# Performance work log

Measured on AMD Instinct MI355X. Metric: run time of the kernel, lower is better.

## Reference

```python
import jax, jax.numpy as jnp
import numpy as np
import math

ALPHA = 2.0  # spikingjelly surrogate.ATan default alpha
TAU = 2.0
MEM_DECAY = math.exp(-1.0 / TAU)
ADAPT_STRENGTH = 0.1
TARGET_RATE = 0.02
THR_MIN = 0.5
N_HEAD = 4

@jax.custom_vjp
def spike_fn(x):
    # Heaviside forward, ATan surrogate backward
    return (x >= 0.0).astype(x.dtype)

def _spike_fwd(x):
    return spike_fn(x), x

def _spike_bwd(x, g):
    return (g * (ALPHA / 2.0) / (1.0 + (jnp.pi / 2.0 * ALPHA * x) ** 2),)

spike_fn.defvjp(_spike_fwd, _spike_bwd)

def lif_step(x, v_mem, thr):
    # thr is a buffer in torch (updated under no_grad): no grad flows to it
    thr_c = jax.lax.stop_gradient(thr)
    v_pot = v_mem * MEM_DECAY + x
    spike = spike_fn(v_pot - thr_c)
    v_new = v_pot * (1.0 - jax.lax.stop_gradient(spike))
    err = jax.lax.stop_gradient(jnp.mean(spike)) - TARGET_RATE
    thr_new = jnp.maximum(thr_c + ADAPT_STRENGTH * err, THR_MIN)
    return spike, v_new, thr_new

def setup_inputs() -> dict:
    key = jax.random.key(0)
    ks = jax.random.split(key, 10)
    B, T, S, D, DS = 8, 16, 256, 512, 64
    x = jax.random.normal(ks[0], (B, T, S, D), jnp.float32)
    A = jax.random.normal(ks[1], (DS, DS), jnp.float32)
    C = jax.random.normal(ks[2], (D, DS), jnp.float32)
    s = 1.0 / math.sqrt(DS)
    Wq = jax.random.uniform(ks[3], (DS, DS), jnp.float32, -s, s)
    bq = jax.random.uniform(ks[4], (DS,), jnp.float32, -s, s)
    sd = 1.0 / math.sqrt(D)
    Wkv = jax.random.uniform(ks[5], (2 * DS, D), jnp.float32, -sd, sd)
    bkv = jax.random.uniform(ks[6], (2 * DS,), jnp.float32, -sd, sd)
    Wo = jax.random.uniform(ks[7], (DS, DS), jnp.float32, -s, s)
    bo = jax.random.uniform(ks[8], (DS,), jnp.float32, -s, s)
    thr_s0 = jnp.full((DS,), 1.0, jnp.float32)
    thr_o0 = jnp.full((D,), 1.0, jnp.float32)
    return {"x": x, "A": A, "C": C, "Wq": Wq, "bq": bq, "Wkv": Wkv,
            "bkv": bkv, "Wo": Wo, "bo": bo, "thr_s0": thr_s0, "thr_o0": thr_o0}

def reference(x, A, C, Wq, bq, Wkv, bkv, Wo, bo, thr_s0, thr_o0):
    B, T, S, D = x.shape
    DS = A.shape[0]
    H = N_HEAD
    dh = DS // H
    N = B * S
    scale = 1.0 / math.sqrt(dh)
    h0 = jnp.zeros((B, S, DS), x.dtype)
    sv0 = jnp.zeros((B, S, DS), x.dtype)
    ov0 = jnp.zeros((B, S, D), x.dtype)

    def step(carry, x_t):
        h, sv, ov, ts, to = carry
        state_transition = h @ A.T                              # (B,S,DS)
        q = (h @ Wq.T + bq).reshape(N, H, dh).transpose(1, 0, 2)   # (H,N,dh)
        kv = x_t @ Wkv.T + bkv                                  # (B,S,2*DS)
        k = kv[..., :DS].reshape(N, H, dh).transpose(1, 0, 2)   # (H,N,dh)
        v = kv[..., DS:].reshape(N, H, dh).transpose(1, 0, 2)   # (H,N,dh)
        scores = jnp.einsum('hnd,hmd->hnm', q, k) * scale       # (H,N,N)
        w = jax.nn.softmax(scores, axis=-1)
        att = jnp.einsum('hnm,hmd->hnd', w, v)                  # (H,N,dh)
        att = att.transpose(1, 0, 2).reshape(B, S, DS)
        state_update = state_transition + att @ Wo.T + bo
        h2, sv2, ts2 = lif_step(state_update, sv, ts)
        output_potential = h2 @ C.T                             # (B,S,D)
        out, ov2, to2 = lif_step(output_potential, ov, to)
        return (h2, sv2, ov2, ts2, to2), out

    _, outs = jax.lax.scan(step, (h0, sv0, ov0, thr_s0, thr_o0),
                           jnp.moveaxis(x, 1, 0))               # outs: (T,B,S,D)
    return jnp.moveaxis(outs, 0, 1)                             # (B,T,S,D)
```

## Files before the change

### kernel.cpp

```cpp
#include <hip/hip_runtime.h>
#include <math.h>


#define NTOK   2048
#define TSTEPS 16
#define NSPLIT 32

#define MEMDECAY ((float)0.6065306597126334)
#define SCALE    0.25f

#define OFF_KV   ((size_t)0)
#define OFF_PACC ((size_t)4194304)
#define OFF_OV   ((size_t)8388608)
#define OFF_H    ((size_t)9437184)
#define OFF_SV   ((size_t)9568256)
#define OFF_Q    ((size_t)9699328)
#define OFF_PM   ((size_t)9830400)
#define OFF_PL   ((size_t)10092544)
#define OFF_CT   ((size_t)10354688)
#define OFF_CNT  ((size_t)10387456)
#define OFF_WT   ((size_t)10387488)

__global__ __launch_bounds__(256) void init_kernel(const float* __restrict__ bq,
                                                   const float* __restrict__ C,
                                                   const float* __restrict__ Wkv,
                                                   float* __restrict__ ws) {
  int i = blockIdx.x * 256 + threadIdx.x;
  if (i < 327680) {
    float4 z = {0.f, 0.f, 0.f, 0.f};
    ((float4*)(ws + OFF_OV))[i] = z;
    return;
  }
  i -= 327680;
  if (i < 131072) { ws[OFF_Q + i] = bq[i & 63]; return; }
  i -= 131072;
  if (i < 32768) {
    int k = i >> 9, c = i & 511;
    ws[OFF_CT + i] = C[c * 64 + k];
    return;
  }
  i -= 32768;
  if (i < 65536) {
    int k = i >> 7, o = i & 127;
    ws[OFF_WT + i] = Wkv[o * 512 + k];
    return;
  }
  i -= 65536;
  if (i < 32) ((int*)(ws + OFF_CNT))[i] = 0;
}

__global__ __launch_bounds__(256) void kv_gemm_kernel(const float* __restrict__ x,
                                                      const float* __restrict__ wkt,
                                                      const float* __restrict__ bkv,
                                                      float* __restrict__ ws) {
  __shared__ float xs[64 * 68];
  __shared__ float wt[64 * 136];
  const int tid = threadIdx.x;
  const int mbase = blockIdx.x * 64;
  const int rg = tid >> 4;
  const int cg = tid & 15;

  float acc[4][8];
#pragma unroll
  for (int i = 0; i < 4; ++i)
#pragma unroll
    for (int j = 0; j < 8; ++j) acc[i][j] = 0.f;

  for (int kt = 0; kt < 8; ++kt) {
    const int kb = kt * 64;
#pragma unroll
    for (int p = 0; p < 4; ++p) {
      int e = tid + p * 256;
      int r = e >> 4, kq = e & 15;
      int row = mbase + r;
      int t_ = row >> 11, n = row & 2047;
      int b = n >> 8, s = n & 255;
      float4 v = *(const float4*)(x + (size_t)((b * 16 + t_) * 256 + s) * 512 + kb + kq * 4);
      *(float4*)(xs + r * 68 + kq * 4) = v;
    }
#pragma unroll
    for (int p = 0; p < 8; ++p) {
      int e = tid + p * 256;
      int k = e >> 5, cq = e & 31;
      float4 v = *(const float4*)(wkt + (size_t)(kb + k) * 128 + cq * 4);
      *(float4*)(wt + k * 136 + cq * 4) = v;
    }
    __syncthreads();
#pragma unroll 2
    for (int kq = 0; kq < 16; ++kq) {
      float4 a0 = *(const float4*)(xs + (rg * 4 + 0) * 68 + kq * 4);
      float4 a1 = *(const float4*)(xs + (rg * 4 + 1) * 68 + kq * 4);
      float4 a2 = *(const float4*)(xs + (rg * 4 + 2) * 68 + kq * 4);
      float4 a3 = *(const float4*)(xs + (rg * 4 + 3) * 68 + kq * 4);
      const float* ap[4] = {(const float*)&a0, (const float*)&a1,
                            (const float*)&a2, (const float*)&a3};
#pragma unroll
      for (int kk = 0; kk < 3 + 1; ++kk) {
        const float* wp = wt + (kq * 4 + kk) * 136 + cg * 8;
        float4 b0 = *(const float4*)(wp);
        float4 b1 = *(const float4*)(wp + 4);
#pragma unroll
        for (int i = 0; i < 4; ++i) {
          float av = ap[i][kk];
          acc[i][0] += av * b0.x; acc[i][1] += av * b0.y;
          acc[i][2] += av * b0.z; acc[i][3] += av * b0.w;
          acc[i][4] += av * b1.x; acc[i][5] += av * b1.y;
          acc[i][6] += av * b1.z; acc[i][7] += av * b1.w;
        }
      }
    }
    __syncthreads();
  }
  float4 bb0 = *(const float4*)(bkv + cg * 8);
  float4 bb1 = *(const float4*)(bkv + cg * 8 + 4);
  float* kvout = ws + OFF_KV;
#pragma unroll
  for (int i = 0; i < 4; ++i) {
    float* op = kvout + (size_t)(mbase + rg * 4 + i) * 128 + cg * 8;
    float4 v0; v0.x = acc[i][0] + bb0.x; v0.y = acc[i][1] + bb0.y;
    v0.z = acc[i][2] + bb0.z; v0.w = acc[i][3] + bb0.w;
    float4 v1; v1.x = acc[i][4] + bb1.x; v1.y = acc[i][5] + bb1.y;
    v1.z = acc[i][6] + bb1.z; v1.w = acc[i][7] + bb1.w;
    *(float4*)(op) = v0;
    *(float4*)(op + 4) = v1;
  }
}

__device__ __forceinline__ void attp_body(int blk, int tid, int t,
                                          const float* __restrict__ kvbase,
                                          const float* __restrict__ qbuf,
                                          float* __restrict__ pm,
                                          float* __restrict__ pl,
                                          float* __restrict__ pacc,
                                          float* smem) {
  const int head = blk & 3;
  const int qt = (blk >> 2) & 3;
  const int sp = blk >> 4;
  float* kl = smem;
  float* vl = smem + 1024;
  const float* kvt = kvbase + (size_t)t * NTOK * 128;
  {
    int key = tid >> 2, dq = tid & 3;
    const float* base = kvt + (size_t)(sp * 64 + key) * 128 + head * 16;
    float4 kk = ((const float4*)base)[dq];
    float4 vv = ((const float4*)(base + 64))[dq];
    ((float4*)kl)[key * 4 + dq] = kk;
    ((float4*)vl)[key * 4 + dq] = vv;
  }
  const int i0 = qt * 512 + tid;
  const int i1 = i0 + 256;
  float q0[16], q1[16];
  {
    const float4* qp0 = (const float4*)(qbuf + (size_t)i0 * 64 + head * 16);
    const float4* qp1 = (const float4*)(qbuf + (size_t)i1 * 64 + head * 16);
#pragma unroll
    for (int r = 0; r < 4; ++r) {
      float4 a = qp0[r];
      q0[4 * r] = a.x; q0[4 * r + 1] = a.y; q0[4 * r + 2] = a.z; q0[4 * r + 3] = a.w;
      float4 b = qp1[r];
      q1[4 * r] = b.x; q1[4 * r + 1] = b.y; q1[4 * r + 2] = b.z; q1[4 * r + 3] = b.w;
    }
  }
  __syncthreads();
  float m0 = -INFINITY, l0 = 0.f, m1 = -INFINITY, l1 = 0.f;
  float acc0[16], acc1[16];
#pragma unroll
  for (int d = 0; d < 16; ++d) { acc0[d] = 0.f; acc1[d] = 0.f; }

#pragma unroll
  for (int ch = 0; ch < 4; ++ch) {
    float sc0[16], sc1[16];
#pragma unroll
    for (int j = 0; j < 16; ++j) {
      const float* kp = kl + (ch * 16 + j) * 16;
      float s0 = 0.f, s1 = 0.f;
#pragma unroll
      for (int d = 0; d < 16; ++d) { float kv_ = kp[d]; s0 += q0[d] * kv_; s1 += q1[d] * kv_; }
      sc0[j] = s0 * SCALE; sc1[j] = s1 * SCALE;
    }
    float mb0 = sc0[0], mb1 = sc1[0];
#pragma unroll
    for (int j = 1; j < 16; ++j) { mb0 = fmaxf(mb0, sc0[j]); mb1 = fmaxf(mb1, sc1[j]); }
    float mn0 = fmaxf(m0, mb0), mn1 = fmaxf(m1, mb1);
    float r0 = expf(m0 - mn0), r1 = expf(m1 - mn1);
    l0 *= r0; l1 *= r1;
#pragma unroll
    for (int d = 0; d < 16; ++d) { acc0[d] *= r0; acc1[d] *= r1; }
#pragma unroll
    for (int j = 0; j < 16; ++j) {
      float w0 = expf(sc0[j] - mn0), w1 = expf(sc1[j] - mn1);
      l0 += w0; l1 += w1; sc0[j] = w0; sc1[j] = w1;
    }
#pragma unroll
    for (int j = 0; j < 16; ++j) {
      const float* vp = vl + (ch * 16 + j) * 16;
      float w0 = sc0[j], w1 = sc1[j];
#pragma unroll
      for (int d = 0; d < 16; ++d) { float vv = vp[d]; acc0[d] += w0 * vv; acc1[d] += w1 * vv; }
    }
    m0 = mn0; m1 = mn1;
  }
  const int pbase = (head * NSPLIT + sp) * NTOK;
  pm[pbase + i0] = m0; pm[pbase + i1] = m1;
  pl[pbase + i0] = l0; pl[pbase + i1] = l1;
  float4* pa0 = (float4*)(pacc + (size_t)(pbase + i0) * 16);
  float4* pa1 = (float4*)(pacc + (size_t)(pbase + i1) * 16);
#pragma unroll
  for (int r = 0; r < 4; ++r) {
    float4 v0; v0.x = acc0[4 * r]; v0.y = acc0[4 * r + 1]; v0.z = acc0[4 * r + 2]; v0.w = acc0[4 * r + 3];
    pa0[r] = v0;
    float4 v1; v1.x = acc1[4 * r]; v1.y = acc1[4 * r + 1]; v1.z = acc1[4 * r + 2]; v1.w = acc1[4 * r + 3];
    pa1[r] = v1;
  }
}

__global__ __launch_bounds__(256) void attp_kernel(int t, float* __restrict__ ws) {
  __shared__ float smem[2048];
  attp_body(blockIdx.x, threadIdx.x, t, ws + OFF_KV, ws + OFF_Q,
            ws + OFF_PM, ws + OFF_PL, ws + OFF_PACC, smem);
}

__global__ __launch_bounds__(256) void combine_lifs_kernel(
    int t, const float* __restrict__ A, const float* __restrict__ Wq,
    const float* __restrict__ bq, const float* __restrict__ Wo,
    const float* __restrict__ bo, const float* __restrict__ thr_s0,
    float* __restrict__ ws) {
  __shared__ float As[64 * 68], Wqs[64 * 68], Wos[64 * 68];
  __shared__ float att_s[4][64], hv_s[4][64], sp_s[4][64];
  __shared__ int scnt;
  const int tid = threadIdx.x;
#pragma unroll
  for (int p = 0; p < 4; ++p) {
    int e = tid + p * 256;
    int c = e >> 4, kq = e & 15;
    *(float4*)(As + c * 68 + kq * 4)  = *(const float4*)(A + c * 64 + kq * 4);
    *(float4*)(Wqs + c * 68 + kq * 4) = *(const float4*)(Wq + c * 64 + kq * 4);
    *(float4*)(Wos + c * 68 + kq * 4) = *(const float4*)(Wo + c * 64 + kq * 4);
  }
  if (tid == 0) scnt = 0;

  const float* pm = ws + OFF_PM;
  const float* pl = ws + OFF_PL;
  const float* pacc = ws + OFF_PACC;
  float* h = ws + OFF_H;
  float* sv = ws + OFF_SV;
  float* qb = ws + OFF_Q;
  int* cnt = (int*)(ws + OFF_CNT);

  const int lane = tid & 63, w = tid >> 6;
  const int n = blockIdx.x * 4 + w;
  const int head = lane >> 4, d = lane & 15;
  const int pb = head * NSPLIT * NTOK + n;

  float mstar = -INFINITY;
  for (int s = 0; s < NSPLIT; ++s) mstar = fmaxf(mstar, pm[pb + s * NTOK]);
  float lst = 0.f, av = 0.f;
  for (int s = 0; s < NSPLIT; ++s) {
    float e = expf(pm[pb + s * NTOK] - mstar);
    lst += e * pl[pb + s * NTOK];
    av += e * pacc[(size_t)(pb + s * NTOK) * 16 + d];
  }
  att_s[w][lane] = av / lst;
  float hv = h[n * 64 + lane];
  hv_s[w][lane] = hv;
  __syncthreads();

  const float* Ar = As + lane * 68;
  const float* Wor = Wos + lane * 68;
  float st = 0.f, wo = 0.f;
#pragma unroll
  for (int kq = 0; kq < 16; ++kq) {
    float4 wa = *(const float4*)(Ar + kq * 4);
    float4 wb = *(const float4*)(Wor + kq * 4);
    float4 hb = *(const float4*)(&hv_s[w][kq * 4]);
    float4 ab = *(const float4*)(&att_s[w][kq * 4]);
    st += hb.x * wa.x; st += hb.y * wa.y; st += hb.z * wa.z; st += hb.w * wa.w;
    wo += ab.x * wb.x; wo += ab.y * wb.y; wo += ab.z * wb.z; wo += ab.w * wb.w;
  }
  float su = st + wo + bo[lane];

  float thr = thr_s0[0];
  const float inv = 1.0f / 131072.0f;
  for (int i = 0; i < t; ++i) {
    float mean = (float)cnt[i] * inv;
    thr = fmaxf(thr + 0.1f * (mean - 0.02f), 0.5f);
  }
  float svo = sv[n * 64 + lane];
  float vpot = svo * MEMDECAY + su;
  float spk = (vpot >= thr) ? 1.f : 0.f;
  h[n * 64 + lane] = spk;
  sv[n * 64 + lane] = vpot * (1.f - spk);
  sp_s[w][lane] = spk;
  unsigned long long sm = __ballot(spk > 0.5f);

  const float* Wqr = Wqs + lane * 68;
  float qv = 0.f;
#pragma unroll
  for (int kq = 0; kq < 16; ++kq) {
    float4 wq = *(const float4*)(Wqr + kq * 4);
    float4 sb = *(const float4*)(&sp_s[w][kq * 4]);
    qv += sb.x * wq.x; qv += sb.y * wq.y; qv += sb.z * wq.z; qv += sb.w * wq.w;
  }
  qb[n * 64 + lane] = qv + bq[lane];

  if (lane == 0) atomicAdd(&scnt, __popcll(sm));
  __syncthreads();
  if (tid == 0) atomicAdd(&cnt[t], scnt);
}

__global__ __launch_bounds__(256) void fused_out_attp_kernel(
    int t, const float* __restrict__ thr_o0, float* __restrict__ out,
    float* __restrict__ ws) {
  __shared__ float smem[64 * 66 + 64 * 68];
  __shared__ int scnt;
  const int blk = blockIdx.x;
  if (blk >= 256) {
    attp_body(blk - 256, threadIdx.x, t + 1, ws + OFF_KV, ws + OFF_Q,
              ws + OFF_PM, ws + OFF_PL, ws + OFF_PACC, smem);
    return;
  }
  const int tid = threadIdx.x;
  const int nt = blk >> 3;
  const int ct = blk & 7;
  float* hs = smem;
  float* cts = smem + 64 * 66;
  const float* h = ws + OFF_H;
  const float* Ct = ws + OFF_CT;
  float* ov = ws + OFF_OV;
  int* cnt = (int*)(ws + OFF_CNT);

#pragma unroll
  for (int p = 0; p < 4; ++p) {
    int e = tid + p * 256;
    int r = e >> 4, kq = e & 15;
    float4 v = *(const float4*)(h + (size_t)(nt * 64 + r) * 64 + kq * 4);
    float* dd = hs + r * 66 + kq * 4;
    dd[0] = v.x; dd[1] = v.y; dd[2] = v.z; dd[3] = v.w;
  }
#pragma unroll
  for (int p = 0; p < 4; ++p) {
    int e = tid + p * 256;
    int k = e >> 4, cq = e & 15;
    float4 v = *(const float4*)(Ct + (size_t)k * 512 + ct * 64 + cq * 4);
    float* dd = cts + k * 68 + cq * 4;
    dd[0] = v.x; dd[1] = v.y; dd[2] = v.z; dd[3] = v.w;
  }
  if (tid == 0) scnt = 0;
  __syncthreads();

  const int tr = tid >> 4, tc = tid & 15;
  float acc[4][4];
#pragma unroll
  for (int i = 0; i < 4; ++i)
#pragma unroll
    for (int j = 0; j < 4; ++j) acc[i][j] = 0.f;

#pragma unroll 4
  for (int k = 0; k < 64; ++k) {
    float hv[4];
#pragma unroll
    for (int i = 0; i < 4; ++i) hv[i] = hs[(tr + i * 16) * 66 + k];
    const float* cp = cts + k * 68 + tc * 4;
    float c0 = cp[0], c1 = cp[1], c2 = cp[2], c3 = cp[3];
#pragma unroll
    for (int i = 0; i < 4; ++i) {
      acc[i][0] += hv[i] * c0;
      acc[i][1] += hv[i] * c1;
      acc[i][2] += hv[i] * c2;
      acc[i][3] += hv[i] * c3;
    }
  }

  float thr = thr_o0[0];
  const float inv = 1.0f / 1048576.0f;
  for (int i = 0; i < t; ++i) {
    float mean = (float)cnt[16 + i] * inv;
    thr = fmaxf(thr + 0.1f * (mean - 0.02f), 0.5f);
  }

  int mycount = 0;
#pragma unroll
  for (int i = 0; i < 4; ++i) {
    int n = nt * 64 + tr + i * 16;
    int b = n >> 8, s = n & 255;
    size_t coff = (size_t)ct * 64 + tc * 4;
    float* ovp = ov + (size_t)n * 512 + coff;
    float* outp = out + ((size_t)(b * 16 + t) * 256 + s) * 512 + coff;
    float4 o = *(float4*)ovp;
    float v0 = o.x * MEMDECAY + acc[i][0];
    float v1 = o.y * MEMDECAY + acc[i][1];
    float v2 = o.z * MEMDECAY + acc[i][2];
    float v3 = o.w * MEMDECAY + acc[i][3];
    float s0 = (v0 >= thr) ? 1.f : 0.f;
    float s1 = (v1 >= thr) ? 1.f : 0.f;
    float s2 = (v2 >= thr) ? 1.f : 0.f;
    float s3 = (v3 >= thr) ? 1.f : 0.f;
    float4 sp; sp.x = s0; sp.y = s1; sp.z = s2; sp.w = s3;
    *(float4*)outp = sp;
    float4 nv; nv.x = v0 * (1.f - s0); nv.y = v1 * (1.f - s1);
    nv.z = v2 * (1.f - s2); nv.w = v3 * (1.f - s3);
    *(float4*)ovp = nv;
    mycount += (int)(s0 + s1 + s2 + s3);
  }
  atomicAdd(&scnt, mycount);
  __syncthreads();
  if (tid == 0) atomicAdd(&cnt[16 + t], scnt);
}

extern "C" void kernel_launch(void* const* d_in, const int* in_sizes, int n_in,
                              void* d_out, int out_size, void* d_ws, size_t ws_size,
                              hipStream_t stream) {
  const float* x    = (const float*)d_in[0];
  const float* A    = (const float*)d_in[1];
  const float* C    = (const float*)d_in[2];
  const float* Wq   = (const float*)d_in[3];
  const float* bq   = (const float*)d_in[4];
  const float* Wkv  = (const float*)d_in[5];
  const float* bkv  = (const float*)d_in[6];
  const float* Wo   = (const float*)d_in[7];
  const float* bo   = (const float*)d_in[8];
  const float* th_s = (const float*)d_in[9];
  const float* th_o = (const float*)d_in[10];
  float* out = (float*)d_out;
  float* ws = (float*)d_ws;

  init_kernel<<<dim3(2177), dim3(256), 0, stream>>>(bq, C, Wkv, ws);
  kv_gemm_kernel<<<dim3(512), dim3(256), 0, stream>>>(x, ws + OFF_WT, bkv, ws);
  attp_kernel<<<dim3(512), dim3(256), 0, stream>>>(0, ws);
  for (int t = 0; t < TSTEPS; ++t) {
    combine_lifs_kernel<<<dim3(512), dim3(256), 0, stream>>>(t, A, Wq, bq, Wo, bo, th_s, ws);
    int g = (t < TSTEPS - 1) ? 768 : 256;
    fused_out_attp_kernel<<<dim3(g), dim3(256), 0, stream>>>(t, th_o, out, ws);
  }
}
```

Measured before the change: 1.002 ms.

## Halve attention key splits, one query per thread, reorder KV projection columns

The split-KV attention partial kernel now uses 16 splits of 128 keys instead of 32 splits of 64 keys. Each thread handles one query instead of two, with 8 query tiles instead of 4, so the grid size stays the same. This halves the partial max/sum/accumulator traffic written per step and read by the combine kernel, at the cost of double the key length per block and twice the shared memory. The KV projection kernel also changes which output columns each thread owns, writing K and V halves with cg*4 strides, and the combine loops are unrolled.

```diff
diff --git a/kernel.cpp b/kernel.cpp
--- a/kernel.cpp
+++ b/kernel.cpp
@@ -4,22 +4,22 @@
 
 #define NTOK   2048
 #define TSTEPS 16
-#define NSPLIT 32
+#define NSPLIT 16
 
 #define MEMDECAY ((float)0.6065306597126334)
 #define SCALE    0.25f
 
 #define OFF_KV   ((size_t)0)
 #define OFF_PACC ((size_t)4194304)
-#define OFF_OV   ((size_t)8388608)
-#define OFF_H    ((size_t)9437184)
-#define OFF_SV   ((size_t)9568256)
-#define OFF_Q    ((size_t)9699328)
-#define OFF_PM   ((size_t)9830400)
-#define OFF_PL   ((size_t)10092544)
-#define OFF_CT   ((size_t)10354688)
-#define OFF_CNT  ((size_t)10387456)
-#define OFF_WT   ((size_t)10387488)
+#define OFF_OV   ((size_t)6291456)
+#define OFF_H    ((size_t)7340032)
+#define OFF_SV   ((size_t)7471104)
+#define OFF_Q    ((size_t)7602176)
+#define OFF_PM   ((size_t)7733248)
+#define OFF_PL   ((size_t)7864320)
+#define OFF_CT   ((size_t)7995392)
+#define OFF_CNT  ((size_t)8028160)
+#define OFF_WT   ((size_t)8028192)
 
 __global__ __launch_bounds__(256) void init_kernel(const float* __restrict__ bq,
                                                    const float* __restrict__ C,
@@ -95,10 +95,10 @@
       const float* ap[4] = {(const float*)&a0, (const float*)&a1,
                             (const float*)&a2, (const float*)&a3};
 #pragma unroll
-      for (int kk = 0; kk < 3 + 1; ++kk) {
-        const float* wp = wt + (kq * 4 + kk) * 136 + cg * 8;
-        float4 b0 = *(const float4*)(wp);
-        float4 b1 = *(const float4*)(wp + 4);
+      for (int kk = 0; kk < 4; ++kk) {
+        const float* wp = wt + (kq * 4 + kk) * 136;
+        float4 b0 = *(const float4*)(wp + cg * 4);
+        float4 b1 = *(const float4*)(wp + 64 + cg * 4);
 #pragma unroll
         for (int i = 0; i < 4; ++i) {
           float av = ap[i][kk];
@@ -111,18 +111,18 @@
     }
     __syncthreads();
   }
-  float4 bb0 = *(const float4*)(bkv + cg * 8);
-  float4 bb1 = *(const float4*)(bkv + cg * 8 + 4);
+  float4 bb0 = *(const float4*)(bkv + cg * 4);
+  float4 bb1 = *(const float4*)(bkv + 64 + cg * 4);
   float* kvout = ws + OFF_KV;
 #pragma unroll
   for (int i = 0; i < 4; ++i) {
-    float* op = kvout + (size_t)(mbase + rg * 4 + i) * 128 + cg * 8;
+    float* op = kvout + (size_t)(mbase + rg * 4 + i) * 128;
     float4 v0; v0.x = acc[i][0] + bb0.x; v0.y = acc[i][1] + bb0.y;
     v0.z = acc[i][2] + bb0.z; v0.w = acc[i][3] + bb0.w;
     float4 v1; v1.x = acc[i][4] + bb1.x; v1.y = acc[i][5] + bb1.y;
     v1.z = acc[i][6] + bb1.z; v1.w = acc[i][7] + bb1.w;
-    *(float4*)(op) = v0;
-    *(float4*)(op + 4) = v1;
+    *(float4*)(op + cg * 4) = v0;
+    *(float4*)(op + 64 + cg * 4) = v1;
   }
 }
 
@@ -134,88 +134,81 @@
                                           float* __restrict__ pacc,
                                           float* smem) {
   const int head = blk & 3;
-  const int qt = (blk >> 2) & 3;
-  const int sp = blk >> 4;
+  const int qt = (blk >> 2) & 7;
+  const int sp = blk >> 5;
   float* kl = smem;
-  float* vl = smem + 1024;
+  float* vl = smem + 2048;
   const float* kvt = kvbase + (size_t)t * NTOK * 128;
-  {
-    int key = tid >> 2, dq = tid & 3;
-    const float* base = kvt + (size_t)(sp * 64 + key) * 128 + head * 16;
-    float4 kk = ((const float4*)base)[dq];
-    float4 vv = ((const float4*)(base + 64))[dq];
-    ((float4*)kl)[key * 4 + dq] = kk;
-    ((float4*)vl)[key * 4 + dq] = vv;
-  }
-  const int i0 = qt * 512 + tid;
-  const int i1 = i0 + 256;
-  float q0[16], q1[16];
+#pragma unroll
+  for (int p = 0; p < 2; ++p) {
+    int e = tid + p * 256;
+    int key = e >> 2, dq = e & 3;
+    const float* base = kvt + (size_t)(sp * 128 + key) * 128 + head * 16;
+    ((float4*)kl)[key * 4 + dq] = ((const float4*)base)[dq];
+    ((float4*)vl)[key * 4 + dq] = ((const float4*)(base + 64))[dq];
+  }
+  const int i0 = qt * 256 + tid;
+  float q0[16];
   {
     const float4* qp0 = (const float4*)(qbuf + (size_t)i0 * 64 + head * 16);
-    const float4* qp1 = (const float4*)(qbuf + (size_t)i1 * 64 + head * 16);
 #pragma unroll
     for (int r = 0; r < 4; ++r) {
       float4 a = qp0[r];
       q0[4 * r] = a.x; q0[4 * r + 1] = a.y; q0[4 * r + 2] = a.z; q0[4 * r + 3] = a.w;
-      float4 b = qp1[r];
-      q1[4 * r] = b.x; q1[4 * r + 1] = b.y; q1[4 * r + 2] = b.z; q1[4 * r + 3] = b.w;
     }
   }
   __syncthreads();
-  float m0 = -INFINITY, l0 = 0.f, m1 = -INFINITY, l1 = 0.f;
-  float acc0[16], acc1[16];
-#pragma unroll
-  for (int d = 0; d < 16; ++d) { acc0[d] = 0.f; acc1[d] = 0.f; }
-
-#pragma unroll
-  for (int ch = 0; ch < 4; ++ch) {
-    float sc0[16], sc1[16];
+  float m0 = -INFINITY, l0 = 0.f;
+  float acc0[16];
+#pragma unroll
+  for (int d = 0; d < 16; ++d) acc0[d] = 0.f;
+
+  for (int ch = 0; ch < 8; ++ch) {
+    float sc0[16];
 #pragma unroll
     for (int j = 0; j < 16; ++j) {
       const float* kp = kl + (ch * 16 + j) * 16;
-      float s0 = 0.f, s1 = 0.f;
-#pragma unroll
-      for (int d = 0; d < 16; ++d) { float kv_ = kp[d]; s0 += q0[d] * kv_; s1 += q1[d] * kv_; }
-      sc0[j] = s0 * SCALE; sc1[j] = s1 * SCALE;
-    }
-    float mb0 = sc0[0], mb1 = sc1[0];
-#pragma unroll
-    for (int j = 1; j < 16; ++j) { mb0 = fmaxf(mb0, sc0[j]); mb1 = fmaxf(mb1, sc1[j]); }
-    float mn0 = fmaxf(m0, mb0), mn1 = fmaxf(m1, mb1);
-    float r0 = expf(m0 - mn0), r1 = expf(m1 - mn1);
-    l0 *= r0; l1 *= r1;
-#pragma unroll
-    for (int d = 0; d < 16; ++d) { acc0[d] *= r0; acc1[d] *= r1; }
+      float s0 = 0.f;
+#pragma unroll
+      for (int d = 0; d < 16; ++d) s0 += q0[d] * kp[d];
+      sc0[j] = s0 * SCALE;
+    }
+    float mb0 = sc0[0];
+#pragma unroll
+    for (int j = 1; j < 16; ++j) mb0 = fmaxf(mb0, sc0[j]);
+    float mn0 = fmaxf(m0, mb0);
+    float r0 = expf(m0 - mn0);
+    l0 *= r0;
+#pragma unroll
+    for (int d = 0; d < 16; ++d) acc0[d] *= r0;
 #pragma unroll
     for (int j = 0; j < 16; ++j) {
-      float w0 = expf(sc0[j] - mn0), w1 = expf(sc1[j] - mn1);
-      l0 += w0; l1 += w1; sc0[j] = w0; sc1[j] = w1;
+      float w0 = expf(sc0[j] - mn0);
+      l0 += w0; sc0[j] = w0;
     }
 #pragma unroll
     for (int j = 0; j < 16; ++j) {
       const float* vp = vl + (ch * 16 + j) * 16;
-      float w0 = sc0[j], w1 = sc1[j];
-#pragma unroll
-      for (int d = 0; d < 16; ++d) { float vv = vp[d]; acc0[d] += w0 * vv; acc1[d] += w1 * vv; }
-    }
-    m0 = mn0; m1 = mn1;
+      float w0 = sc0[j];
+#pragma unroll
+      for (int d = 0; d < 16; ++d) acc0[d] += w0 * vp[d];
+    }
+    m0 = mn0;
   }
   const int pbase = (head * NSPLIT + sp) * NTOK;
-  pm[pbase + i0] = m0; pm[pbase + i1] = m1;
-  pl[pbase + i0] = l0; pl[pbase + i1] = l1;
+  pm[pbase + i0] = m0;
+  pl[pbase + i0] = l0;
   float4* pa0 = (float4*)(pacc + (size_t)(pbase + i0) * 16);
-  float4* pa1 = (float4*)(pacc + (size_t)(pbase + i1) * 16);
 #pragma unroll
   for (int r = 0; r < 4; ++r) {
-    float4 v0; v0.x = acc0[4 * r]; v0.y = acc0[4 * r + 1]; v0.z = acc0[4 * r + 2]; v0.w = acc0[4 * r + 3];
+    float4 v0; v0.x = acc0[4 * r]; v0.y = acc0[4 * r + 1];
+    v0.z = acc0[4 * r + 2]; v0.w = acc0[4 * r + 3];
     pa0[r] = v0;
-    float4 v1; v1.x = acc1[4 * r]; v1.y = acc1[4 * r + 1]; v1.z = acc1[4 * r + 2]; v1.w = acc1[4 * r + 3];
-    pa1[r] = v1;
   }
 }
 
 __global__ __launch_bounds__(256) void attp_kernel(int t, float* __restrict__ ws) {
-  __shared__ float smem[2048];
+  __shared__ float smem[4096];
   attp_body(blockIdx.x, threadIdx.x, t, ws + OFF_KV, ws + OFF_Q,
             ws + OFF_PM, ws + OFF_PL, ws + OFF_PACC, smem);
 }
@@ -253,8 +246,10 @@
   const int pb = head * NSPLIT * NTOK + n;
 
   float mstar = -INFINITY;
+#pragma unroll
   for (int s = 0; s < NSPLIT; ++s) mstar = fmaxf(mstar, pm[pb + s * NTOK]);
   float lst = 0.f, av = 0.f;
+#pragma unroll
   for (int s = 0; s < NSPLIT; ++s) {
     float e = expf(pm[pb + s * NTOK] - mstar);
     lst += e * pl[pb + s * NTOK];
```

Result: slower. 1.051 ms (+4.9%).
